# Kernel optimization log

Measured on AMD Instinct MI355X. Metric: run time of the kernel, lower is better.

## Reference

```python
import jax, jax.numpy as jnp
import numpy as np

N = 50000
K = 4
D_IN = 256
D_OUT = 64
E = 800000

def setup_inputs() -> dict:
    key = jax.random.key(0)
    k1, k2, k3, k4, k5 = jax.random.split(key, 5)
    x = jax.random.normal(k1, (N, K, D_IN), dtype=jnp.float32)
    weight = jax.random.normal(k2, (D_IN, D_OUT), dtype=jnp.float32) * (1.0 / np.sqrt(D_IN))
    adj_rows = jax.random.randint(k3, (E,), 0, N, dtype=jnp.int32)
    adj_cols = jax.random.randint(k4, (E,), 0, N, dtype=jnp.int32)
    adj_vals = jax.random.uniform(k5, (E,), dtype=jnp.float32)
    return {"x": x, "weight": weight, "adj_rows": adj_rows, "adj_cols": adj_cols, "adj_vals": adj_vals}

def reference(x, weight, adj_rows, adj_cols, adj_vals):
    # x: [N, K, D_in]; weight: [D_in, D_out]
    # dropout p=0.0 / eval mode -> identity
    # support = x @ W for every sample k, vectorized over K
    support = jnp.einsum('nkd,df->nkf', x, weight)          # [N, K, D_out]
    # sparse adj matmul: out[r] += vals[e] * support[cols[e]]
    msgs = adj_vals[:, None, None] * support[adj_cols]       # [E, K, D_out]
    out = jax.ops.segment_sum(msgs, adj_rows, num_segments=N)  # [N, K, D_out]
    return jax.nn.relu(out)
```

## Files before the change

### kernel.cpp

```cpp
#include <hip/hip_runtime.h>
#include <stdint.h>

#define D_IN   256
#define D_OUT  64
#define KHEADS 4
#define ROWLEN 256
#define GBM    128
#define LDW    264
#define WBT_B  (64 * LDW * 2)
#define CAP    128

typedef __attribute__((ext_vector_type(8))) short bf16x8;
typedef __attribute__((ext_vector_type(4))) float f32x4;

__device__ __forceinline__ unsigned cvt_pk_bf16(float lo, float hi) {
  unsigned r;
  asm("v_cvt_pk_bf16_f32 %0, %1, %2" : "=v"(r) : "v"(lo), "v"(hi));
  return r;
}

__device__ __forceinline__ bf16x8 pack8(float4 a, float4 b) {
  union { unsigned u[4]; bf16x8 v; } r;
  r.u[0] = cvt_pk_bf16(a.x, a.y);
  r.u[1] = cvt_pk_bf16(a.z, a.w);
  r.u[2] = cvt_pk_bf16(b.x, b.y);
  r.u[3] = cvt_pk_bf16(b.z, b.w);
  return r.v;
}

__global__ __launch_bounds__(256) void prep_w(const float* __restrict__ W,
                                              unsigned short* __restrict__ WbT) {
  int idx = blockIdx.x * 256 + threadIdx.x;
  int n  = idx >> 6;
  int k0 = (idx & 63) << 2;
  float w0 = W[(size_t)(k0 + 0) * D_OUT + n];
  float w1 = W[(size_t)(k0 + 1) * D_OUT + n];
  float w2 = W[(size_t)(k0 + 2) * D_OUT + n];
  float w3 = W[(size_t)(k0 + 3) * D_OUT + n];
  unsigned p0 = cvt_pk_bf16(w0, w1);
  unsigned p1 = cvt_pk_bf16(w2, w3);
  *(uint2*)&WbT[(size_t)n * LDW + k0] = make_uint2(p0, p1);
}

__device__ __forceinline__ void gemm_body(const float* __restrict__ X,
                                          const unsigned short* __restrict__ WbT,
                                          signed char* __restrict__ Sq,
                                          float* __restrict__ scaleArr,
                                          int M, int Nnodes, int gb) {
  __shared__ __align__(16) unsigned short lWt[64 * LDW];
  const int t    = threadIdx.x;
  const int wave = t >> 6;
  const int lane = t & 63;
  const int q    = lane >> 4;
  const int l16  = lane & 15;
  const long row0 = (long)gb * GBM;

  {
    const uint4* __restrict__ src = (const uint4*)WbT;
    uint4* dst = (uint4*)lWt;
#pragma unroll
    for (int r2 = 0; r2 < 9; ++r2) {
      int slot = t + r2 * 256;
      if (slot < WBT_B / 16) dst[slot] = src[slot];
    }
  }
  __syncthreads();

  long r0 = row0 + wave * 32 + l16;       if (r0 > (long)M - 1) r0 = M - 1;
  long r1 = row0 + wave * 32 + 16 + l16;  if (r1 > (long)M - 1) r1 = M - 1;
  const float* __restrict__ x0 = X + r0 * D_IN + q * 8;
  const float* __restrict__ x1 = X + r1 * D_IN + q * 8;

  f32x4 acc[2][4];
#pragma unroll
  for (int rb = 0; rb < 2; ++rb)
#pragma unroll
    for (int cb = 0; cb < 4; ++cb) acc[rb][cb] = (f32x4){0.f, 0.f, 0.f, 0.f};

  float4 c00 = *(const float4*)(x0);
  float4 c01 = *(const float4*)(x0 + 4);
  float4 c10 = *(const float4*)(x1);
  float4 c11 = *(const float4*)(x1 + 4);
#pragma unroll
  for (int s = 0; s < 8; ++s) {
    float4 n00, n01, n10, n11;
    if (s < 7) {
      const float* p0 = x0 + (s + 1) * 32;
      const float* p1 = x1 + (s + 1) * 32;
      n00 = *(const float4*)(p0); n01 = *(const float4*)(p0 + 4);
      n10 = *(const float4*)(p1); n11 = *(const float4*)(p1 + 4);
    }
    bf16x8 a0 = pack8(c00, c01);
    bf16x8 a1 = pack8(c10, c11);
    const unsigned short* wb = &lWt[l16 * LDW + s * 32 + q * 8];
#pragma unroll
    for (int cb = 0; cb < 4; ++cb) {
      bf16x8 b = *(const bf16x8*)(wb + cb * 16 * LDW);
      acc[0][cb] = __builtin_amdgcn_mfma_f32_16x16x32_bf16(a0, b, acc[0][cb], 0, 0, 0);
      acc[1][cb] = __builtin_amdgcn_mfma_f32_16x16x32_bf16(a1, b, acc[1][cb], 0, 0, 0);
    }
    if (s < 7) { c00 = n00; c01 = n01; c10 = n10; c11 = n11; }
  }

  float nm0 = 0.f, nm1 = 0.f;
#pragma unroll
  for (int cb = 0; cb < 4; ++cb)
#pragma unroll
    for (int reg = 0; reg < 4; ++reg) {
      nm0 = fmaxf(nm0, fabsf(acc[0][cb][reg]));
      nm1 = fmaxf(nm1, fabsf(acc[1][cb][reg]));
    }
#pragma unroll
  for (int d = 1; d < 16; d <<= 1) {
    nm0 = fmaxf(nm0, __shfl_xor(nm0, d, 64));
    nm1 = fmaxf(nm1, __shfl_xor(nm1, d, 64));
  }
  const float inv0 = (nm0 > 0.f) ? 127.f / nm0 : 0.f;
  const float inv1 = (nm1 > 0.f) ? 127.f / nm1 : 0.f;
  const int node_base = gb * 32 + wave * 8;
  if (l16 == 0) {
    int n0 = node_base + q;
    int n1 = node_base + 4 + q;
    if (n0 < Nnodes) scaleArr[n0] = nm0 / 127.f;
    if (n1 < Nnodes) scaleArr[n1] = nm1 / 127.f;
  }
#pragma unroll
  for (int rb = 0; rb < 2; ++rb) {
    const float inv = rb ? inv1 : inv0;
#pragma unroll
    for (int cb = 0; cb < 4; ++cb)
#pragma unroll
      for (int reg = 0; reg < 4; ++reg) {
        long r = row0 + wave * 32 + rb * 16 + q * 4 + reg;
        if (r < M) {
          int qi = (int)rintf(acc[rb][cb][reg] * inv);
          Sq[r * D_OUT + cb * 16 + l16] = (signed char)qi;
        }
      }
  }
}

__device__ __forceinline__ void place_body(const int* __restrict__ rows,
                                           const int* __restrict__ cols,
                                           const float* __restrict__ vals,
                                           int* __restrict__ cnt,
                                           uint2* __restrict__ ecv, int E, int pb) {
  int e = pb * 256 + threadIdx.x;
  if (e < E) {
    int r = rows[e];
    int c = cols[e];
    float v = vals[e];
    int pos = atomicAdd(&cnt[r], 1);
    if (pos < CAP)
      ecv[((size_t)r << 7) + pos] = make_uint2((unsigned)c, __float_as_uint(v));
  }
}

__global__ __launch_bounds__(256) void fused_phase1(
    const float* __restrict__ X, const unsigned short* __restrict__ WbT,
    signed char* __restrict__ Sq, float* __restrict__ scaleArr,
    const int* __restrict__ rows, const int* __restrict__ cols,
    const float* __restrict__ vals, int* __restrict__ cnt,
    uint2* __restrict__ ecv, int M, int Nnodes, int E, int G, int P) {
  const int bid = blockIdx.x;
  const int g = bid / 3, r3 = bid - 3 * g;
  if (r3 == 0) {
    if (g < G) gemm_body(X, WbT, Sq, scaleArr, M, Nnodes, g);
  } else {
    int pb = 2 * g + r3 - 1;
    if (pb < P) place_body(rows, cols, vals, cnt, ecv, E, pb);
  }
}

__global__ __launch_bounds__(256) void gather_kernel(const int* __restrict__ Sqi,
                                                     const float* __restrict__ scaleArr,
                                                     const int* __restrict__ cnt,
                                                     const uint2* __restrict__ ecv,
                                                     float* __restrict__ out, int n) {
  const int lane = threadIdx.x & 63;
  const int r = blockIdx.x * 4 + (threadIdx.x >> 6);
  if (r >= n) return;
  int deg = cnt[r];
  if (deg > CAP) deg = CAP;
  const uint2* __restrict__ bucket = ecv + ((size_t)r << 7);

  unsigned long long bl =
      __builtin_nontemporal_load((const unsigned long long*)bucket + lane);
  unsigned mc = (lane < deg) ? (unsigned)bl : 0u;
  float    mv = (lane < deg) ? __uint_as_float((unsigned)(bl >> 32)) * scaleArr[mc] : 0.f;

  float4 a0 = make_float4(0.f, 0.f, 0.f, 0.f);
  float4 a1 = a0, a2 = a0, a3 = a0;
  const int d0 = deg < 64 ? deg : 64;
  for (int i = 0; i < d0; i += 8) {
    unsigned cc[8]; float vv[8]; int ww[8];
#pragma unroll
    for (int u = 0; u < 8; ++u) {
      int e = i + u;
      int ec = e < d0 ? e : d0 - 1;
      cc[u] = __shfl(mc, ec);
      float vraw = __shfl(mv, ec);
      vv[u] = (e < d0) ? vraw : 0.f;
    }
#pragma unroll
    for (int u = 0; u < 8; ++u) ww[u] = Sqi[(size_t)cc[u] * 64 + lane];
#pragma unroll
    for (int u = 0; u < 8; ++u) {
      float4& a = ((u & 3) == 0) ? a0 : (((u & 3) == 1) ? a1 : (((u & 3) == 2) ? a2 : a3));
      const float v = vv[u];
      const int   w = ww[u];
      a.x += v * (float)(w << 24 >> 24);
      a.y += v * (float)(w << 16 >> 24);
      a.z += v * (float)(w <<  8 >> 24);
      a.w += v * (float)(w >> 24);
    }
  }
  if (deg > 64) {
    uint2 b1 = bucket[64 + lane];
    unsigned mc1 = (64 + lane < deg) ? b1.x : 0u;
    float    mv1 = (64 + lane < deg) ? __uint_as_float(b1.y) * scaleArr[mc1] : 0.f;
    for (int e = 64; e < deg; ++e) {
      unsigned c = __shfl(mc1, e - 64);
      float    v = __shfl(mv1, e - 64);
      int w = Sqi[(size_t)c * 64 + lane];
      a0.x += v * (float)(w << 24 >> 24); a0.y += v * (float)(w << 16 >> 24);
      a0.z += v * (float)(w <<  8 >> 24); a0.w += v * (float)(w >> 24);
    }
  }
  f32x4 res;
  res[0] = fmaxf(a0.x + a1.x + a2.x + a3.x, 0.f);
  res[1] = fmaxf(a0.y + a1.y + a2.y + a3.y, 0.f);
  res[2] = fmaxf(a0.z + a1.z + a2.z + a3.z, 0.f);
  res[3] = fmaxf(a0.w + a1.w + a2.w + a3.w, 0.f);
  __builtin_nontemporal_store(res, (f32x4*)&out[(size_t)r * ROWLEN + (lane << 2)]);
}

extern "C" void kernel_launch(void* const* d_in, const int* in_sizes, int n_in,
                              void* d_out, int out_size, void* d_ws, size_t ws_size,
                              hipStream_t stream) {
  const float* x    = (const float*)d_in[0];
  const float* w    = (const float*)d_in[1];
  const int*   rows = (const int*)d_in[2];
  const int*   cols = (const int*)d_in[3];
  const float* vals = (const float*)d_in[4];
  float* out = (float*)d_out;

  const int E = in_sizes[2];
  const int N = in_sizes[0] / (KHEADS * D_IN);
  const int M = N * KHEADS;

  char* ws = (char*)d_ws;
  size_t o = 0;
  signed char* Sq = (signed char*)(ws + o); o += (size_t)M * D_OUT;
  o = (o + 15) & ~(size_t)15;
  float* scaleArr = (float*)(ws + o); o += (size_t)N * sizeof(float);
  o = (o + 15) & ~(size_t)15;
  int* cnt = (int*)(ws + o); o += (size_t)N * sizeof(int);
  o = (o + 63) & ~(size_t)63;
  unsigned short* WbT = (unsigned short*)(ws + o); o += WBT_B;
  o = (o + 15) & ~(size_t)15;
  uint2* ecv = (uint2*)(ws + o);

  hipMemsetAsync(cnt, 0, (size_t)N * sizeof(int), stream);

  const int G = (M + GBM - 1) / GBM;
  const int P = (E + 255) / 256;
  prep_w<<<16, 256, 0, stream>>>(w, WbT);
  fused_phase1<<<3 * G, 256, 0, stream>>>(x, WbT, Sq, scaleArr, rows, cols, vals,
                                          cnt, ecv, M, N, E, G, P);
  gather_kernel<<<(N + 3) / 4, 256, 0, stream>>>((const int*)Sq, scaleArr, cnt, ecv, out, N);
}
```

Measured before the change: 365.1 us.

## Store quantized support head-major and split gather per head; fuse placement into GEMM blocks

Each GEMM block now also scatters 512 edges into the per-row buckets, replacing the interleaved three-way block split. The int8 support is written head-major ([head][node][64]), so each head's slice is a smaller contiguous region that gather waves can hit in cache. The gather launches one wave per (row, head). Each wave processes four edges at once, using 16 lanes per edge, then reduces across lane groups with shuffles. In exchange, the bucket and scale loads are repeated once per head, and the final cross-lane reduction adds extra shuffle work.

```diff
diff --git a/kernel.cpp b/kernel.cpp
--- a/kernel.cpp
+++ b/kernel.cpp
@@ -9,6 +9,7 @@
 #define LDW    264
 #define WBT_B  (64 * LDW * 2)
 #define CAP    128
+#define EPB    512
 
 typedef __attribute__((ext_vector_type(8))) short bf16x8;
 typedef __attribute__((ext_vector_type(4))) float f32x4;
@@ -42,29 +43,48 @@
   *(uint2*)&WbT[(size_t)n * LDW + k0] = make_uint2(p0, p1);
 }
 
-__device__ __forceinline__ void gemm_body(const float* __restrict__ X,
-                                          const unsigned short* __restrict__ WbT,
-                                          signed char* __restrict__ Sq,
-                                          float* __restrict__ scaleArr,
-                                          int M, int Nnodes, int gb) {
+__global__ __launch_bounds__(256) void fused_gemm_place(
+    const float* __restrict__ X, const unsigned short* __restrict__ WbT,
+    signed char* __restrict__ SqH, float* __restrict__ scaleArr,
+    const int* __restrict__ rows, const int* __restrict__ cols,
+    const float* __restrict__ vals, int* __restrict__ cnt,
+    uint2* __restrict__ ecv, int M, int Nnodes, int E) {
   __shared__ __align__(16) unsigned short lWt[64 * LDW];
   const int t    = threadIdx.x;
+  const int g    = blockIdx.x;
+
+  {
+    int base = g * EPB + t;
+#pragma unroll
+    for (int u = 0; u < 2; ++u) {
+      int e = base + u * 256;
+      if (e < E) {
+        int r = rows[e];
+        int c = cols[e];
+        float v = vals[e];
+        int pos = atomicAdd(&cnt[r], 1);
+        if (pos < CAP)
+          ecv[((size_t)r << 7) + pos] = make_uint2((unsigned)c, __float_as_uint(v));
+      }
+    }
+  }
+
+  {
+    const uint4* __restrict__ src = (const uint4*)WbT;
+    uint4* dst = (uint4*)lWt;
+#pragma unroll
+    for (int r2 = 0; r2 < 9; ++r2) {
+      int slot = t + r2 * 256;
+      if (slot < WBT_B / 16) dst[slot] = src[slot];
+    }
+  }
+  __syncthreads();
+
   const int wave = t >> 6;
   const int lane = t & 63;
   const int q    = lane >> 4;
   const int l16  = lane & 15;
-  const long row0 = (long)gb * GBM;
-
-  {
-    const uint4* __restrict__ src = (const uint4*)WbT;
-    uint4* dst = (uint4*)lWt;
-#pragma unroll
-    for (int r2 = 0; r2 < 9; ++r2) {
-      int slot = t + r2 * 256;
-      if (slot < WBT_B / 16) dst[slot] = src[slot];
-    }
-  }
-  __syncthreads();
+  const long row0 = (long)g * GBM;
 
   long r0 = row0 + wave * 32 + l16;       if (r0 > (long)M - 1) r0 = M - 1;
   long r1 = row0 + wave * 32 + 16 + l16;  if (r1 > (long)M - 1) r1 = M - 1;
@@ -117,7 +137,7 @@
   }
   const float inv0 = (nm0 > 0.f) ? 127.f / nm0 : 0.f;
   const float inv1 = (nm1 > 0.f) ? 127.f / nm1 : 0.f;
-  const int node_base = gb * 32 + wave * 8;
+  const int node_base = g * 32 + wave * 8;
   if (l16 == 0) {
     int n0 = node_base + q;
     int n1 = node_base + 4 + q;
@@ -134,105 +154,84 @@
         long r = row0 + wave * 32 + rb * 16 + q * 4 + reg;
         if (r < M) {
           int qi = (int)rintf(acc[rb][cb][reg] * inv);
-          Sq[r * D_OUT + cb * 16 + l16] = (signed char)qi;
+          int node = (int)(r >> 2);
+          int head = (int)(r & 3);
+          SqH[((size_t)head * Nnodes + node) * 64 + cb * 16 + l16] = (signed char)qi;
         }
       }
   }
 }
 
-__device__ __forceinline__ void place_body(const int* __restrict__ rows,
-                                           const int* __restrict__ cols,
-                                           const float* __restrict__ vals,
-                                           int* __restrict__ cnt,
-                                           uint2* __restrict__ ecv, int E, int pb) {
-  int e = pb * 256 + threadIdx.x;
-  if (e < E) {
-    int r = rows[e];
-    int c = cols[e];
-    float v = vals[e];
-    int pos = atomicAdd(&cnt[r], 1);
-    if (pos < CAP)
-      ecv[((size_t)r << 7) + pos] = make_uint2((unsigned)c, __float_as_uint(v));
-  }
-}
-
-__global__ __launch_bounds__(256) void fused_phase1(
-    const float* __restrict__ X, const unsigned short* __restrict__ WbT,
-    signed char* __restrict__ Sq, float* __restrict__ scaleArr,
-    const int* __restrict__ rows, const int* __restrict__ cols,
-    const float* __restrict__ vals, int* __restrict__ cnt,
-    uint2* __restrict__ ecv, int M, int Nnodes, int E, int G, int P) {
-  const int bid = blockIdx.x;
-  const int g = bid / 3, r3 = bid - 3 * g;
-  if (r3 == 0) {
-    if (g < G) gemm_body(X, WbT, Sq, scaleArr, M, Nnodes, g);
-  } else {
-    int pb = 2 * g + r3 - 1;
-    if (pb < P) place_body(rows, cols, vals, cnt, ecv, E, pb);
-  }
-}
-
-__global__ __launch_bounds__(256) void gather_kernel(const int* __restrict__ Sqi,
-                                                     const float* __restrict__ scaleArr,
-                                                     const int* __restrict__ cnt,
-                                                     const uint2* __restrict__ ecv,
-                                                     float* __restrict__ out, int n) {
+__global__ __launch_bounds__(256) void gather_kernel(
+    const signed char* __restrict__ SqH, const float* __restrict__ scaleArr,
+    const int* __restrict__ cnt, const uint2* __restrict__ ecv,
+    float* __restrict__ out, int n, int bph) {
+  const int bid  = blockIdx.x;
+  const int head = bid / bph;
+  const int rb   = (bid - head * bph) * 4 + (threadIdx.x >> 6);
+  if (rb >= n) return;
   const int lane = threadIdx.x & 63;
-  const int r = blockIdx.x * 4 + (threadIdx.x >> 6);
-  if (r >= n) return;
-  int deg = cnt[r];
+  const int e2   = lane >> 4;
+  const int d16  = lane & 15;
+  int deg = cnt[rb];
   if (deg > CAP) deg = CAP;
-  const uint2* __restrict__ bucket = ecv + ((size_t)r << 7);
-
-  unsigned long long bl =
-      __builtin_nontemporal_load((const unsigned long long*)bucket + lane);
-  unsigned mc = (lane < deg) ? (unsigned)bl : 0u;
-  float    mv = (lane < deg) ? __uint_as_float((unsigned)(bl >> 32)) * scaleArr[mc] : 0.f;
-
-  float4 a0 = make_float4(0.f, 0.f, 0.f, 0.f);
-  float4 a1 = a0, a2 = a0, a3 = a0;
-  const int d0 = deg < 64 ? deg : 64;
-  for (int i = 0; i < d0; i += 8) {
-    unsigned cc[8]; float vv[8]; int ww[8];
-#pragma unroll
-    for (int u = 0; u < 8; ++u) {
-      int e = i + u;
-      int ec = e < d0 ? e : d0 - 1;
-      cc[u] = __shfl(mc, ec);
-      float vraw = __shfl(mv, ec);
-      vv[u] = (e < d0) ? vraw : 0.f;
-    }
-#pragma unroll
-    for (int u = 0; u < 8; ++u) ww[u] = Sqi[(size_t)cc[u] * 64 + lane];
-#pragma unroll
-    for (int u = 0; u < 8; ++u) {
-      float4& a = ((u & 3) == 0) ? a0 : (((u & 3) == 1) ? a1 : (((u & 3) == 2) ? a2 : a3));
-      const float v = vv[u];
-      const int   w = ww[u];
-      a.x += v * (float)(w << 24 >> 24);
-      a.y += v * (float)(w << 16 >> 24);
-      a.z += v * (float)(w <<  8 >> 24);
-      a.w += v * (float)(w >> 24);
-    }
+  const uint2* __restrict__ bucket = ecv + ((size_t)rb << 7);
+
+  unsigned long long bl = *((const unsigned long long*)bucket + lane);
+  const unsigned mc = (lane < deg) ? (unsigned)bl : 0u;
+  const float    mv = (lane < deg)
+      ? __uint_as_float((unsigned)(bl >> 32)) * scaleArr[mc] : 0.f;
+
+  const int* __restrict__ Sh = (const int*)SqH + (size_t)head * (size_t)n * 16;
+
+  float4 aA = make_float4(0.f, 0.f, 0.f, 0.f);
+  float4 aB = aA;
+  const int d0  = deg < 64 ? deg : 64;
+  const int nd0 = (d0 + 7) & ~7;
+  for (int i = 0; i < nd0; i += 8) {
+    const int eA = i + e2;
+    const int eB = i + 4 + e2;
+    const unsigned cA = __shfl(mc, eA);
+    const unsigned cB = __shfl(mc, eB);
+    const float    vA = __shfl(mv, eA);
+    const float    vB = __shfl(mv, eB);
+    const int wA = Sh[(size_t)cA * 16 + d16];
+    const int wB = Sh[(size_t)cB * 16 + d16];
+    aA.x += vA * (float)(wA << 24 >> 24); aA.y += vA * (float)(wA << 16 >> 24);
+    aA.z += vA * (float)(wA <<  8 >> 24); aA.w += vA * (float)(wA >> 24);
+    aB.x += vB * (float)(wB << 24 >> 24); aB.y += vB * (float)(wB << 16 >> 24);
+    aB.z += vB * (float)(wB <<  8 >> 24); aB.w += vB * (float)(wB >> 24);
   }
   if (deg > 64) {
-    uint2 b1 = bucket[64 + lane];
-    unsigned mc1 = (64 + lane < deg) ? b1.x : 0u;
-    float    mv1 = (64 + lane < deg) ? __uint_as_float(b1.y) * scaleArr[mc1] : 0.f;
-    for (int e = 64; e < deg; ++e) {
-      unsigned c = __shfl(mc1, e - 64);
-      float    v = __shfl(mv1, e - 64);
-      int w = Sqi[(size_t)c * 64 + lane];
-      a0.x += v * (float)(w << 24 >> 24); a0.y += v * (float)(w << 16 >> 24);
-      a0.z += v * (float)(w <<  8 >> 24); a0.w += v * (float)(w >> 24);
-    }
-  }
-  f32x4 res;
-  res[0] = fmaxf(a0.x + a1.x + a2.x + a3.x, 0.f);
-  res[1] = fmaxf(a0.y + a1.y + a2.y + a3.y, 0.f);
-  res[2] = fmaxf(a0.z + a1.z + a2.z + a3.z, 0.f);
-  res[3] = fmaxf(a0.w + a1.w + a2.w + a3.w, 0.f);
-  __builtin_nontemporal_store(res, (f32x4*)&out[(size_t)r * ROWLEN + (lane << 2)]);
+    unsigned long long bl1 = *((const unsigned long long*)bucket + 64 + lane);
+    const unsigned mc1 = (64 + lane < deg) ? (unsigned)bl1 : 0u;
+    const float    mv1 = (64 + lane < deg)
+        ? __uint_as_float((unsigned)(bl1 >> 32)) * scaleArr[mc1] : 0.f;
+    const int ndt = (deg + 3) & ~3;
+    for (int i = 64; i < ndt; i += 4) {
+      const int idx = i + e2 - 64;
+      const unsigned cA = __shfl(mc1, idx);
+      const float    vA = __shfl(mv1, idx);
+      const int wA = Sh[(size_t)cA * 16 + d16];
+      aA.x += vA * (float)(wA << 24 >> 24); aA.y += vA * (float)(wA << 16 >> 24);
+      aA.z += vA * (float)(wA <<  8 >> 24); aA.w += vA * (float)(wA >> 24);
+    }
+  }
+  float4 a;
+  a.x = aA.x + aB.x; a.y = aA.y + aB.y; a.z = aA.z + aB.z; a.w = aA.w + aB.w;
+  a.x += __shfl_xor(a.x, 16, 64); a.y += __shfl_xor(a.y, 16, 64);
+  a.z += __shfl_xor(a.z, 16, 64); a.w += __shfl_xor(a.w, 16, 64);
+  a.x += __shfl_xor(a.x, 32, 64); a.y += __shfl_xor(a.y, 32, 64);
+  a.z += __shfl_xor(a.z, 32, 64); a.w += __shfl_xor(a.w, 32, 64);
+  if (e2 == 0) {
+    f32x4 res;
+    res[0] = fmaxf(a.x, 0.f);
+    res[1] = fmaxf(a.y, 0.f);
+    res[2] = fmaxf(a.z, 0.f);
+    res[3] = fmaxf(a.w, 0.f);
+    __builtin_nontemporal_store(
+        res, (f32x4*)&out[(size_t)rb * ROWLEN + head * 64 + (d16 << 2)]);
+  }
 }
 
 extern "C" void kernel_launch(void* const* d_in, const int* in_sizes, int n_in,
@@ -251,7 +250,7 @@
 
   char* ws = (char*)d_ws;
   size_t o = 0;
-  signed char* Sq = (signed char*)(ws + o); o += (size_t)M * D_OUT;
+  signed char* SqH = (signed char*)(ws + o); o += (size_t)M * D_OUT;
   o = (o + 15) & ~(size_t)15;
   float* scaleArr = (float*)(ws + o); o += (size_t)N * sizeof(float);
   o = (o + 15) & ~(size_t)15;
@@ -263,10 +262,13 @@
 
   hipMemsetAsync(cnt, 0, (size_t)N * sizeof(int), stream);
 
-  const int G = (M + GBM - 1) / GBM;
-  const int P = (E + 255) / 256;
+  int G = (M + GBM - 1) / GBM;
+  const int Ge = (E + EPB - 1) / EPB;
+  if (Ge > G) G = Ge;
   prep_w<<<16, 256, 0, stream>>>(w, WbT);
-  fused_phase1<<<3 * G, 256, 0, stream>>>(x, WbT, Sq, scaleArr, rows, cols, vals,
-                                          cnt, ecv, M, N, E, G, P);
-  gather_kernel<<<(N + 3) / 4, 256, 0, stream>>>((const int*)Sq, scaleArr, cnt, ecv, out, N);
-}
+  fused_gemm_place<<<G, 256, 0, stream>>>(x, WbT, SqH, scaleArr, rows, cols,
+                                          vals, cnt, ecv, M, N, E);
+  const int bph = (N + 3) / 4;
+  gather_kernel<<<bph * KHEADS, 256, 0, stream>>>(SqH, scaleArr, cnt, ecv,
+                                                  out, N, bph);
+}
```

Result: slower. 419.3 us (+14.9%).

## Read bf16 weights from global/L2 instead of LDS and simplify gather tails

Applied to the files above, without the earlier changes.

The GEMM blocks no longer stage the transposed bf16 weight matrix into shared memory with a barrier. Each lane now reads its B fragments directly from the 32 KB global WbT, which should stay cache-resident, and X rows are streamed with nontemporal loads. The gather loop drops its per-edge bounds clamping, relying on zeroed shuffle values for padded lanes. This removes the LDS fill, the sync and the LDS footprint, which can raise occupancy, at the cost of more global/L1 traffic for weight reads.

```diff
diff --git a/kernel.cpp b/kernel.cpp
--- a/kernel.cpp
+++ b/kernel.cpp
@@ -6,8 +6,6 @@
 #define KHEADS 4
 #define ROWLEN 256
 #define GBM    128
-#define LDW    264
-#define WBT_B  (64 * LDW * 2)
 #define CAP    128
 
 typedef __attribute__((ext_vector_type(8))) short bf16x8;
@@ -19,12 +17,12 @@
   return r;
 }
 
-__device__ __forceinline__ bf16x8 pack8(float4 a, float4 b) {
+__device__ __forceinline__ bf16x8 pack8(f32x4 a, f32x4 b) {
   union { unsigned u[4]; bf16x8 v; } r;
-  r.u[0] = cvt_pk_bf16(a.x, a.y);
-  r.u[1] = cvt_pk_bf16(a.z, a.w);
-  r.u[2] = cvt_pk_bf16(b.x, b.y);
-  r.u[3] = cvt_pk_bf16(b.z, b.w);
+  r.u[0] = cvt_pk_bf16(a[0], a[1]);
+  r.u[1] = cvt_pk_bf16(a[2], a[3]);
+  r.u[2] = cvt_pk_bf16(b[0], b[1]);
+  r.u[3] = cvt_pk_bf16(b[2], b[3]);
   return r.v;
 }
 
@@ -39,37 +37,26 @@
   float w3 = W[(size_t)(k0 + 3) * D_OUT + n];
   unsigned p0 = cvt_pk_bf16(w0, w1);
   unsigned p1 = cvt_pk_bf16(w2, w3);
-  *(uint2*)&WbT[(size_t)n * LDW + k0] = make_uint2(p0, p1);
+  *(uint2*)&WbT[(size_t)n * D_IN + k0] = make_uint2(p0, p1);
 }
 
 __device__ __forceinline__ void gemm_body(const float* __restrict__ X,
                                           const unsigned short* __restrict__ WbT,
                                           signed char* __restrict__ Sq,
                                           float* __restrict__ scaleArr,
-                                          int M, int Nnodes, int gb) {
-  __shared__ __align__(16) unsigned short lWt[64 * LDW];
+                                          int M, int Nnodes, int g) {
   const int t    = threadIdx.x;
   const int wave = t >> 6;
   const int lane = t & 63;
   const int q    = lane >> 4;
   const int l16  = lane & 15;
-  const long row0 = (long)gb * GBM;
-
-  {
-    const uint4* __restrict__ src = (const uint4*)WbT;
-    uint4* dst = (uint4*)lWt;
-#pragma unroll
-    for (int r2 = 0; r2 < 9; ++r2) {
-      int slot = t + r2 * 256;
-      if (slot < WBT_B / 16) dst[slot] = src[slot];
-    }
-  }
-  __syncthreads();
+  const long row0 = (long)g * GBM;
 
   long r0 = row0 + wave * 32 + l16;       if (r0 > (long)M - 1) r0 = M - 1;
   long r1 = row0 + wave * 32 + 16 + l16;  if (r1 > (long)M - 1) r1 = M - 1;
   const float* __restrict__ x0 = X + r0 * D_IN + q * 8;
   const float* __restrict__ x1 = X + r1 * D_IN + q * 8;
+  const unsigned short* __restrict__ wrow = WbT + (size_t)l16 * D_IN + q * 8;
 
   f32x4 acc[2][4];
 #pragma unroll
@@ -77,25 +64,26 @@
 #pragma unroll
     for (int cb = 0; cb < 4; ++cb) acc[rb][cb] = (f32x4){0.f, 0.f, 0.f, 0.f};
 
-  float4 c00 = *(const float4*)(x0);
-  float4 c01 = *(const float4*)(x0 + 4);
-  float4 c10 = *(const float4*)(x1);
-  float4 c11 = *(const float4*)(x1 + 4);
+  f32x4 c00 = __builtin_nontemporal_load((const f32x4*)(x0));
+  f32x4 c01 = __builtin_nontemporal_load((const f32x4*)(x0 + 4));
+  f32x4 c10 = __builtin_nontemporal_load((const f32x4*)(x1));
+  f32x4 c11 = __builtin_nontemporal_load((const f32x4*)(x1 + 4));
 #pragma unroll
   for (int s = 0; s < 8; ++s) {
-    float4 n00, n01, n10, n11;
+    f32x4 n00, n01, n10, n11;
     if (s < 7) {
       const float* p0 = x0 + (s + 1) * 32;
       const float* p1 = x1 + (s + 1) * 32;
-      n00 = *(const float4*)(p0); n01 = *(const float4*)(p0 + 4);
-      n10 = *(const float4*)(p1); n11 = *(const float4*)(p1 + 4);
+      n00 = __builtin_nontemporal_load((const f32x4*)(p0));
+      n01 = __builtin_nontemporal_load((const f32x4*)(p0 + 4));
+      n10 = __builtin_nontemporal_load((const f32x4*)(p1));
+      n11 = __builtin_nontemporal_load((const f32x4*)(p1 + 4));
     }
     bf16x8 a0 = pack8(c00, c01);
     bf16x8 a1 = pack8(c10, c11);
-    const unsigned short* wb = &lWt[l16 * LDW + s * 32 + q * 8];
 #pragma unroll
     for (int cb = 0; cb < 4; ++cb) {
-      bf16x8 b = *(const bf16x8*)(wb + cb * 16 * LDW);
+      bf16x8 b = *(const bf16x8*)(wrow + (size_t)cb * 16 * D_IN + s * 32);
       acc[0][cb] = __builtin_amdgcn_mfma_f32_16x16x32_bf16(a0, b, acc[0][cb], 0, 0, 0);
       acc[1][cb] = __builtin_amdgcn_mfma_f32_16x16x32_bf16(a1, b, acc[1][cb], 0, 0, 0);
     }
@@ -117,7 +105,7 @@
   }
   const float inv0 = (nm0 > 0.f) ? 127.f / nm0 : 0.f;
   const float inv1 = (nm1 > 0.f) ? 127.f / nm1 : 0.f;
-  const int node_base = gb * 32 + wave * 8;
+  const int node_base = g * 32 + wave * 8;
   if (l16 == 0) {
     int n0 = node_base + q;
     int n1 = node_base + 4 + q;
@@ -172,11 +160,10 @@
   }
 }
 
-__global__ __launch_bounds__(256) void gather_kernel(const int* __restrict__ Sqi,
-                                                     const float* __restrict__ scaleArr,
-                                                     const int* __restrict__ cnt,
-                                                     const uint2* __restrict__ ecv,
-                                                     float* __restrict__ out, int n) {
+__global__ __launch_bounds__(256) void gather_kernel(
+    const int* __restrict__ Sqi, const float* __restrict__ scaleArr,
+    const int* __restrict__ cnt, const uint2* __restrict__ ecv,
+    float* __restrict__ out, int n) {
   const int lane = threadIdx.x & 63;
   const int r = blockIdx.x * 4 + (threadIdx.x >> 6);
   if (r >= n) return;
@@ -186,21 +173,20 @@
 
   unsigned long long bl =
       __builtin_nontemporal_load((const unsigned long long*)bucket + lane);
-  unsigned mc = (lane < deg) ? (unsigned)bl : 0u;
-  float    mv = (lane < deg) ? __uint_as_float((unsigned)(bl >> 32)) * scaleArr[mc] : 0.f;
+  const unsigned mc = (lane < deg) ? (unsigned)bl : 0u;
+  const float    mv = (lane < deg)
+      ? __uint_as_float((unsigned)(bl >> 32)) * scaleArr[mc] : 0.f;
 
   float4 a0 = make_float4(0.f, 0.f, 0.f, 0.f);
   float4 a1 = a0, a2 = a0, a3 = a0;
-  const int d0 = deg < 64 ? deg : 64;
-  for (int i = 0; i < d0; i += 8) {
+  const int d0  = deg < 64 ? deg : 64;
+  const int nd0 = (d0 + 7) & ~7;
+  for (int i = 0; i < nd0; i += 8) {
     unsigned cc[8]; float vv[8]; int ww[8];
 #pragma unroll
     for (int u = 0; u < 8; ++u) {
-      int e = i + u;
-      int ec = e < d0 ? e : d0 - 1;
-      cc[u] = __shfl(mc, ec);
-      float vraw = __shfl(mv, ec);
-      vv[u] = (e < d0) ? vraw : 0.f;
+      cc[u] = __shfl(mc, i + u);
+      vv[u] = __shfl(mv, i + u);
     }
 #pragma unroll
     for (int u = 0; u < 8; ++u) ww[u] = Sqi[(size_t)cc[u] * 64 + lane];
@@ -216,13 +202,15 @@
     }
   }
   if (deg > 64) {
-    uint2 b1 = bucket[64 + lane];
-    unsigned mc1 = (64 + lane < deg) ? b1.x : 0u;
-    float    mv1 = (64 + lane < deg) ? __uint_as_float(b1.y) * scaleArr[mc1] : 0.f;
-    for (int e = 64; e < deg; ++e) {
-      unsigned c = __shfl(mc1, e - 64);
-      float    v = __shfl(mv1, e - 64);
-      int w = Sqi[(size_t)c * 64 + lane];
+    unsigned long long bl1 = *((const unsigned long long*)bucket + 64 + lane);
+    const unsigned mc1 = (64 + lane < deg) ? (unsigned)bl1 : 0u;
+    const float    mv1 = (64 + lane < deg)
+        ? __uint_as_float((unsigned)(bl1 >> 32)) * scaleArr[mc1] : 0.f;
+    const int ndt = ((deg - 64) + 7) & ~7;
+    for (int i = 0; i < ndt; ++i) {
+      const unsigned c = __shfl(mc1, i);
+      const float    v = __shfl(mv1, i);
+      const int w = Sqi[(size_t)c * 64 + lane];
       a0.x += v * (float)(w << 24 >> 24); a0.y += v * (float)(w << 16 >> 24);
       a0.z += v * (float)(w <<  8 >> 24); a0.w += v * (float)(w >> 24);
     }
@@ -257,16 +245,18 @@
   o = (o + 15) & ~(size_t)15;
   int* cnt = (int*)(ws + o); o += (size_t)N * sizeof(int);
   o = (o + 63) & ~(size_t)63;
-  unsigned short* WbT = (unsigned short*)(ws + o); o += WBT_B;
+  unsigned short* WbT = (unsigned short*)(ws + o);
+  o += (size_t)D_OUT * D_IN * sizeof(unsigned short);
   o = (o + 15) & ~(size_t)15;
   uint2* ecv = (uint2*)(ws + o);
 
-  hipMemsetAsync(cnt, 0, (size_t)N * sizeof(int), stream);
+  (void)hipMemsetAsync(cnt, 0, (size_t)N * sizeof(int), stream);
 
   const int G = (M + GBM - 1) / GBM;
   const int P = (E + 255) / 256;
   prep_w<<<16, 256, 0, stream>>>(w, WbT);
-  fused_phase1<<<3 * G, 256, 0, stream>>>(x, WbT, Sq, scaleArr, rows, cols, vals,
-                                          cnt, ecv, M, N, E, G, P);
-  gather_kernel<<<(N + 3) / 4, 256, 0, stream>>>((const int*)Sq, scaleArr, cnt, ecv, out, N);
-}
+  fused_phase1<<<3 * G, 256, 0, stream>>>(x, WbT, Sq, scaleArr, rows, cols,
+                                          vals, cnt, ecv, M, N, E, G, P);
+  gather_kernel<<<(N + 3) / 4, 256, 0, stream>>>((const int*)Sq, scaleArr,
+                                                 cnt, ecv, out, N);
+}
```

New measurement: 390.1 us. 1.07x slower.
